# Optimization experiments

Hardware: AMD Instinct MI355X
Metric: run time of the kernel (lower is better)

Reference implementation:

```python
import jax, jax.numpy as jnp
import numpy as np

B, T, S, D, H, DK = 2, 2048, 2048, 1024, 16, 64


def setup_inputs() -> dict:
    key = jax.random.key(0)
    ks = jax.random.split(key, 11)
    s = 1.0 / np.sqrt(D)
    return {
        "query": jax.random.normal(ks[0], (B, T, D), jnp.float32),
        "value": jax.random.normal(ks[1], (B, S, D), jnp.float32),
        "key": jax.random.normal(ks[2], (B, S, D), jnp.float32),
        "Wq": jax.random.normal(ks[3], (D, H, DK), jnp.float32) * s,
        "bq": jnp.zeros((H, DK), jnp.float32),
        "Wk": jax.random.normal(ks[4], (D, H, DK), jnp.float32) * s,
        "bk": jnp.zeros((H, DK), jnp.float32),
        "Wv": jax.random.normal(ks[5], (D, H, DK), jnp.float32) * s,
        "bv": jnp.zeros((H, DK), jnp.float32),
        "Wo": jax.random.normal(ks[6], (H, DK, D), jnp.float32) * (1.0 / np.sqrt(H * DK)),
        "bo": jnp.zeros((D,), jnp.float32),
    }


def reference(query, value, key, Wq, bq, Wk, bk, Wv, bv, Wo, bo):
    # Projections: (B, seq, D) x (D, H, DK) -> (B, seq, H, DK)
    q = jnp.einsum("btd,dhk->bthk", query, Wq) + bq
    k = jnp.einsum("bsd,dhk->bshk", key, Wk) + bk
    v = jnp.einsum("bsd,dhk->bshk", value, Wv) + bv
    # Scaled dot-product attention (keras scales query by 1/sqrt(key_dim))
    q = q * (1.0 / np.sqrt(DK)).astype(np.float32)
    scores = jnp.einsum("bshk,bthk->bhts", k, q)  # (B, H, T, S)
    probs = jax.nn.softmax(scores, axis=-1)
    attn = jnp.einsum("bhts,bshk->bthk", probs, v)  # (B, T, H, DK)
    # Output projection back to model dim
    out = jnp.einsum("bthk,hkd->btd", attn, Wo) + bo
    return out
```

## Files before the change

kernel.cpp:

```cpp
#include <hip/hip_runtime.h>
#include <math.h>

#define BB  2
#define TT  2048
#define SSQ 2048
#define DD  1024
#define HH  16
#define DKK 64
#define MM  (BB*TT)
#define NN  (HH*DKK)

typedef __attribute__((ext_vector_type(8))) short short8;
typedef __attribute__((ext_vector_type(4))) float f32x4;

__device__ __forceinline__ short f2bf(float x) {
    unsigned u = __builtin_bit_cast(unsigned, x);
    unsigned r = (u + 0x7FFFu + ((u >> 16) & 1u)) >> 16;
    return (short)r;
}

__device__ __forceinline__ void glds16(const void* g, void* l) {
    __builtin_amdgcn_global_load_lds(
        (const __attribute__((address_space(1))) void*)g,
        (__attribute__((address_space(3))) void*)l, 16, 0, 0);
}

__global__ __launch_bounds__(256)
void to_bf16_acts(const float* __restrict__ a0, const float* __restrict__ a1,
                  const float* __restrict__ a2,
                  short* __restrict__ o0, short* __restrict__ o1,
                  short* __restrict__ o2)
{
    int z = blockIdx.y;
    const float* in = (z == 0) ? a0 : (z == 1) ? a1 : a2;
    short* out = (z == 0) ? o0 : (z == 1) ? o1 : o2;
    size_t i0 = ((size_t)blockIdx.x * 256 + threadIdx.x) * 8;
    f32x4 f0 = *(const f32x4*)(in + i0);
    f32x4 f1 = *(const f32x4*)(in + i0 + 4);
    short8 v;
#pragma unroll
    for (int j = 0; j < 4; j++) v[j] = f2bf(f0[j]);
#pragma unroll
    for (int j = 0; j < 4; j++) v[4 + j] = f2bf(f1[j]);
    *(short8*)(out + i0) = v;
}

__global__ __launch_bounds__(256)
void wtrans(const float* __restrict__ w0, const float* __restrict__ w1,
            const float* __restrict__ w2, const float* __restrict__ w3,
            short* __restrict__ t0, short* __restrict__ t1,
            short* __restrict__ t2, short* __restrict__ t3)
{
    __shared__ float Ls[64][65];
    int z = blockIdx.z;
    const float* in = (z == 0) ? w0 : (z == 1) ? w1 : (z == 2) ? w2 : w3;
    short* out = (z == 0) ? t0 : (z == 1) ? t1 : (z == 2) ? t2 : t3;
    const int r0 = blockIdx.y * 64, c0 = blockIdx.x * 64;
    const int t = threadIdx.x;
    const int r = t >> 2, c4 = t & 3;

    const float* src = in + (size_t)(r0 + r) * DD + c0 + c4 * 16;
#pragma unroll
    for (int i = 0; i < 4; i++) {
        f32x4 f = *(const f32x4*)(src + i * 4);
#pragma unroll
        for (int j = 0; j < 4; j++) Ls[r][c4 * 16 + i * 4 + j] = f[j];
    }
    __syncthreads();

    short8 va, vb;
#pragma unroll
    for (int j = 0; j < 8; j++) va[j] = f2bf(Ls[c4 * 16 + j][r]);
#pragma unroll
    for (int j = 0; j < 8; j++) vb[j] = f2bf(Ls[c4 * 16 + 8 + j][r]);
    short* dst = out + (size_t)(c0 + r) * DD + r0 + c4 * 16;
    *(short8*)dst = va;
    *(short8*)(dst + 8) = vb;
}

__global__ __launch_bounds__(256)
void vtrans(const short* __restrict__ in, short* __restrict__ out)
{
    __shared__ short Ls[64][72];
    const int bh = blockIdx.y;
    const int t0 = blockIdx.x * 64;
    const int tid = threadIdx.x;
    const int r = tid >> 2, c4 = tid & 3;

    const short* src = in + ((size_t)bh * TT + t0 + r) * DKK + c4 * 16;
    *(short8*)&Ls[r][c4 * 16]     = *(const short8*)(src);
    *(short8*)&Ls[r][c4 * 16 + 8] = *(const short8*)(src + 8);
    __syncthreads();

    short8 a, b;
#pragma unroll
    for (int j = 0; j < 8; j++) a[j] = Ls[c4 * 16 + j][r];
#pragma unroll
    for (int j = 0; j < 8; j++) b[j] = Ls[c4 * 16 + 8 + j][r];
    short* dst = out + ((size_t)bh * DKK + r) * SSQ + t0 + c4 * 16;
    *(short8*)dst = a;
    *(short8*)(dst + 8) = b;
}

__device__ __forceinline__ void gemm_core(const short* __restrict__ A,
                                          const short* __restrict__ Bt,
                                          int m0, int n0,
                                          short* As, short* Bs,
                                          f32x4 (&acc)[4][4])
{
    const int tid = threadIdx.x;
    const int w = tid >> 6, l = tid & 63;
    const int l15 = l & 15, quad = l >> 4;
    const int wm = w >> 1, wn = w & 1;

#pragma unroll
    for (int i = 0; i < 4; i++)
#pragma unroll
        for (int j = 0; j < 4; j++) acc[i][j] = (f32x4){0.f, 0.f, 0.f, 0.f};

    const int r = tid >> 2, cseg = tid & 3;
    const short* gA = A + (size_t)(m0 + r) * DD + cseg * 8;
    const short* gB = Bt + (size_t)(n0 + r) * DD + cseg * 8;
    short* ldsA = As + w * 512;
    short* ldsB = Bs + w * 512;

    for (int k0 = 0; k0 < DD; k0 += 32) {
        glds16(gA + k0,                 ldsA);
        glds16(gA + (size_t)64 * DD + k0, ldsA + 2048);
        glds16(gB + k0,                 ldsB);
        glds16(gB + (size_t)64 * DD + k0, ldsB + 2048);
        __syncthreads();

        short8 bF[4];
#pragma unroll
        for (int ni = 0; ni < 4; ni++)
            bF[ni] = *(const short8*)&Bs[(wn * 64 + ni * 16 + l15) * 32 + quad * 8];
#pragma unroll
        for (int mi = 0; mi < 4; mi++) {
            short8 aF = *(const short8*)&As[(wm * 64 + mi * 16 + l15) * 32 + quad * 8];
#pragma unroll
            for (int ni = 0; ni < 4; ni++)
                acc[mi][ni] = __builtin_amdgcn_mfma_f32_16x16x32_bf16(aF, bF[ni], acc[mi][ni], 0, 0, 0);
        }
        __syncthreads();
    }
}

__global__ __launch_bounds__(256, 3)
void gemm_qkv(const short* __restrict__ Aq, const short* __restrict__ Ak,
              const short* __restrict__ Av,
              const short* __restrict__ Wqt, const short* __restrict__ Wkt,
              const short* __restrict__ Wvt,
              const float* __restrict__ bq, const float* __restrict__ bk,
              const float* __restrict__ bv,
              short* __restrict__ Qb, short* __restrict__ Kb,
              short* __restrict__ Vtmp)
{
    __shared__ short As[128 * 32];
    __shared__ short Bs[128 * 32];
    const int z = blockIdx.z;
    const short* A  = (z == 0) ? Aq : (z == 1) ? Ak : Av;
    const short* Bt = (z == 0) ? Wqt : (z == 1) ? Wkt : Wvt;
    const float* bias = (z == 0) ? bq : (z == 1) ? bk : bv;
    short* dst = (z == 0) ? Qb : (z == 1) ? Kb : Vtmp;
    const int m0 = blockIdx.y * 128, n0 = blockIdx.x * 128;

    f32x4 acc[4][4];
    gemm_core(A, Bt, m0, n0, As, Bs, acc);

    const int tid = threadIdx.x;
    const int w = tid >> 6, l = tid & 63;
    const int l15 = l & 15, quad = l >> 4;
    const int wm = w >> 1, wn = w & 1;
    const float scale = (z == 0) ? 0.1803368801f : 1.0f;

#pragma unroll
    for (int mi = 0; mi < 4; mi++) {
#pragma unroll
        for (int reg = 0; reg < 4; reg++) {
            int m = m0 + wm * 64 + mi * 16 + quad * 4 + reg;
            int b = m >> 11, t = m & 2047;
#pragma unroll
            for (int ni = 0; ni < 4; ni++) {
                int n = n0 + wn * 64 + ni * 16 + l15;
                float vv = (acc[mi][ni][reg] + bias[n]) * scale;
                int h = n >> 6, dk = n & 63;
                dst[((size_t)(b * HH + h) * TT + t) * DKK + dk] = f2bf(vv);
            }
        }
    }
}

__global__ __launch_bounds__(256, 3)
void gemm_out(const short* __restrict__ Ab, const short* __restrict__ Wot,
              const float* __restrict__ bo, float* __restrict__ out)
{
    __shared__ short As[128 * 32];
    __shared__ short Bs[128 * 32];
    const int m0 = blockIdx.y * 128, n0 = blockIdx.x * 128;

    f32x4 acc[4][4];
    gemm_core(Ab, Wot, m0, n0, As, Bs, acc);

    const int tid = threadIdx.x;
    const int w = tid >> 6, l = tid & 63;
    const int l15 = l & 15, quad = l >> 4;
    const int wm = w >> 1, wn = w & 1;

#pragma unroll
    for (int mi = 0; mi < 4; mi++) {
#pragma unroll
        for (int reg = 0; reg < 4; reg++) {
            int m = m0 + wm * 64 + mi * 16 + quad * 4 + reg;
#pragma unroll
            for (int ni = 0; ni < 4; ni++) {
                int n = n0 + wn * 64 + ni * 16 + l15;
                out[(size_t)m * DD + n] = acc[mi][ni][reg] + bo[n];
            }
        }
    }
}

__global__ __launch_bounds__(256, 2)
void attn_mfma(const short* __restrict__ Qb, const short* __restrict__ Kb,
               const short* __restrict__ Vbt, short* __restrict__ Ab)
{
    __shared__ short QPs[128 * 72];
    __shared__ short Ks[64 * 72];
    __shared__ short Vs[64 * 72];

    const int tid = threadIdx.x;
    const int w = tid >> 6, l = tid & 63;
    const int l15 = l & 15, quad = l >> 4;
    const int bh = blockIdx.y;
    const int t0 = blockIdx.x * 128;
    const size_t hb = (size_t)bh * SSQ * DKK;
    const int r = tid >> 2, c4 = tid & 3;

    {
        int r2 = tid >> 1, half = tid & 1;
        const short* g = Qb + hb + (size_t)(t0 + r2) * 64 + half * 32;
        short* s = QPs + r2 * 72 + half * 32;
        *(short8*)(s + 0)  = *(const short8*)(g + 0);
        *(short8*)(s + 8)  = *(const short8*)(g + 8);
        *(short8*)(s + 16) = *(const short8*)(g + 16);
        *(short8*)(s + 24) = *(const short8*)(g + 24);
    }
    __threadfence_block();
    short8 qf[2][2];
#pragma unroll
    for (int mf = 0; mf < 2; mf++)
#pragma unroll
        for (int kk = 0; kk < 2; kk++)
            qf[mf][kk] = *(const short8*)&QPs[(32 * w + 16 * mf + l15) * 72 + kk * 32 + quad * 8];

    const short* gkb = Kb + hb + (size_t)r * 64 + c4 * 16;
    const short* gvb = Vbt + hb + (size_t)r * SSQ + c4 * 16;
    short8 kr0 = *(const short8*)(gkb + 0);
    short8 kr1 = *(const short8*)(gkb + 8);
    short8 vr0 = *(const short8*)(gvb + 0);
    short8 vr1 = *(const short8*)(gvb + 8);

    f32x4 o[2][4];
#pragma unroll
    for (int mf = 0; mf < 2; mf++)
#pragma unroll
        for (int j = 0; j < 4; j++) o[mf][j] = (f32x4){0.f, 0.f, 0.f, 0.f};
    float lsum[2][4];
#pragma unroll
    for (int mf = 0; mf < 2; mf++)
#pragma unroll
        for (int j = 0; j < 4; j++) lsum[mf][j] = 0.f;

    short* sk = Ks + r * 72 + c4 * 16;
    short* sv = Vs + r * 72 + c4 * 16;

    for (int s0 = 0; s0 < SSQ; s0 += 64) {
        __syncthreads();
        *(short8*)(sk + 0) = kr0;
        *(short8*)(sk + 8) = kr1;
        *(short8*)(sv + 0) = vr0;
        *(short8*)(sv + 8) = vr1;
        if (s0 + 64 < SSQ) {
            const short* gk = gkb + (size_t)(s0 + 64) * 64;
            const short* gv = gvb + (s0 + 64);
            kr0 = *(const short8*)(gk + 0);
            kr1 = *(const short8*)(gk + 8);
            vr0 = *(const short8*)(gv + 0);
            vr1 = *(const short8*)(gv + 8);
        }
        __syncthreads();

        f32x4 sc[2][4];
#pragma unroll
        for (int mf = 0; mf < 2; mf++)
#pragma unroll
            for (int j = 0; j < 4; j++) sc[mf][j] = (f32x4){0.f, 0.f, 0.f, 0.f};
#pragma unroll
        for (int kk = 0; kk < 2; kk++) {
#pragma unroll
            for (int np = 0; np < 4; np++) {
                short8 bK = *(const short8*)&Ks[(16 * np + l15) * 72 + kk * 32 + quad * 8];
                sc[0][np] = __builtin_amdgcn_mfma_f32_16x16x32_bf16(qf[0][kk], bK, sc[0][np], 0, 0, 0);
                sc[1][np] = __builtin_amdgcn_mfma_f32_16x16x32_bf16(qf[1][kk], bK, sc[1][np], 0, 0, 0);
            }
        }

#pragma unroll
        for (int mf = 0; mf < 2; mf++) {
            int prow = (32 * w + 16 * mf + quad * 4) * 72 + l15;
#pragma unroll
            for (int reg = 0; reg < 4; reg++) {
                int pr = prow + reg * 72;
#pragma unroll
                for (int np = 0; np < 4; np++) {
                    float p = __builtin_amdgcn_exp2f(sc[mf][np][reg]);
                    QPs[pr + 16 * np] = (short)(__builtin_bit_cast(unsigned, p) >> 16);
                    lsum[mf][reg] += p;
                }
            }
        }
        __threadfence_block();

#pragma unroll
        for (int kk = 0; kk < 2; kk++) {
            short8 aP0 = *(const short8*)&QPs[(32 * w + l15) * 72 + kk * 32 + quad * 8];
            short8 aP1 = *(const short8*)&QPs[(32 * w + 16 + l15) * 72 + kk * 32 + quad * 8];
#pragma unroll
            for (int np = 0; np < 4; np++) {
                short8 bV = *(const short8*)&Vs[(16 * np + l15) * 72 + kk * 32 + quad * 8];
                o[0][np] = __builtin_amdgcn_mfma_f32_16x16x32_bf16(aP0, bV, o[0][np], 0, 0, 0);
                o[1][np] = __builtin_amdgcn_mfma_f32_16x16x32_bf16(aP1, bV, o[1][np], 0, 0, 0);
            }
        }
    }

    const int b = bh >> 4, h = bh & 15;
#pragma unroll
    for (int mf = 0; mf < 2; mf++) {
#pragma unroll
        for (int reg = 0; reg < 4; reg++) {
            float ls = lsum[mf][reg];
            ls += __shfl_xor(ls, 1);
            ls += __shfl_xor(ls, 2);
            ls += __shfl_xor(ls, 4);
            ls += __shfl_xor(ls, 8);
            float inv = 1.f / ls;
            int t = t0 + 32 * w + 16 * mf + quad * 4 + reg;
#pragma unroll
            for (int np = 0; np < 4; np++) {
                Ab[((size_t)(b * TT + t) * HH + h) * DKK + 16 * np + l15] =
                    f2bf(o[mf][np][reg] * inv);
            }
        }
    }
}

extern "C" void kernel_launch(void* const* d_in, const int* in_sizes, int n_in,
                              void* d_out, int out_size, void* d_ws, size_t ws_size,
                              hipStream_t stream)
{
    const float* query = (const float*)d_in[0];
    const float* value = (const float*)d_in[1];
    const float* key   = (const float*)d_in[2];
    const float* Wq    = (const float*)d_in[3];
    const float* bq    = (const float*)d_in[4];
    const float* Wk    = (const float*)d_in[5];
    const float* bk    = (const float*)d_in[6];
    const float* Wv    = (const float*)d_in[7];
    const float* bv    = (const float*)d_in[8];
    const float* Wo    = (const float*)d_in[9];
    const float* bo    = (const float*)d_in[10];
    float* out = (float*)d_out;

    const size_t actE = (size_t)MM * DD;
    const size_t wE   = (size_t)DD * NN;
    short* p = (short*)d_ws;
    short* Aq   = p; p += actE;
    short* Ak   = p; p += actE;
    short* Av   = p; p += actE;
    short* Wqt  = p; p += wE;
    short* Wkt  = p; p += wE;
    short* Wvt  = p; p += wE;
    short* Wot  = p; p += wE;
    short* Qb   = p; p += actE;
    short* Kb   = p; p += actE;
    short* Vtmp = p; p += actE;
    short* Vbt  = p; p += actE;
    short* Ab   = p; p += actE;

    dim3 blk(256);

    to_bf16_acts<<<dim3((unsigned)(actE / 2048), 3), blk, 0, stream>>>(
        query, key, value, Aq, Ak, Av);

    wtrans<<<dim3(16, 16, 4), blk, 0, stream>>>(Wq, Wk, Wv, Wo, Wqt, Wkt, Wvt, Wot);

    gemm_qkv<<<dim3(NN / 128, MM / 128, 3), blk, 0, stream>>>(
        Aq, Ak, Av, Wqt, Wkt, Wvt, bq, bk, bv, Qb, Kb, Vtmp);

    vtrans<<<dim3(TT / 64, BB * HH), blk, 0, stream>>>(Vtmp, Vbt);

    attn_mfma<<<dim3(TT / 128, BB * HH), blk, 0, stream>>>(Qb, Kb, Vbt, Ab);

    gemm_out<<<dim3(DD / 128, MM / 128), blk, 0, stream>>>(Ab, Wot, bo, out);
}
```

Measured before the change: 240.9 us.

## Widen attention KV tile to 128 and use 128x64 tiles for output GEMM

The attention kernel now stages 128 keys and values per iteration instead of 64. This halves the number of barrier-separated loop trips and doubles the K dimension of the P·V MFMA chain, at the cost of more LDS and register pressure. The output projection GEMM switches from 128x128 tiles to 128x64 tiles with its own inlined direct-to-LDS load loop, launching twice as many blocks to fill more CUs. The new layout keeps global loads staged through registers without multi-buffering, so load latency is still only partly hidden.

```diff
diff --git a/kernel.cpp b/kernel.cpp
--- a/kernel.cpp
+++ b/kernel.cpp
@@ -191,30 +191,57 @@
     }
 }
 
-__global__ __launch_bounds__(256, 3)
+__global__ __launch_bounds__(256, 2)
 void gemm_out(const short* __restrict__ Ab, const short* __restrict__ Wot,
               const float* __restrict__ bo, float* __restrict__ out)
 {
     __shared__ short As[128 * 32];
-    __shared__ short Bs[128 * 32];
-    const int m0 = blockIdx.y * 128, n0 = blockIdx.x * 128;
-
-    f32x4 acc[4][4];
-    gemm_core(Ab, Wot, m0, n0, As, Bs, acc);
-
+    __shared__ short Bs[64 * 32];
+    const int m0 = blockIdx.y * 128, n0 = blockIdx.x * 64;
     const int tid = threadIdx.x;
     const int w = tid >> 6, l = tid & 63;
     const int l15 = l & 15, quad = l >> 4;
-    const int wm = w >> 1, wn = w & 1;
-
-#pragma unroll
-    for (int mi = 0; mi < 4; mi++) {
+
+    f32x4 acc[2][4];
+#pragma unroll
+    for (int i = 0; i < 2; i++)
+#pragma unroll
+        for (int j = 0; j < 4; j++) acc[i][j] = (f32x4){0.f, 0.f, 0.f, 0.f};
+
+    const int r = tid >> 2, cseg = tid & 3;
+    const short* gA = Ab + (size_t)(m0 + r) * DD + cseg * 8;
+    const short* gB = Wot + (size_t)(n0 + r) * DD + cseg * 8;
+    short* ldsA = As + w * 512;
+    short* ldsB = Bs + w * 512;
+
+    for (int k0 = 0; k0 < DD; k0 += 32) {
+        glds16(gA + k0,                   ldsA);
+        glds16(gA + (size_t)64 * DD + k0, ldsA + 2048);
+        glds16(gB + k0,                   ldsB);
+        __syncthreads();
+
+        short8 bF[4];
+#pragma unroll
+        for (int ni = 0; ni < 4; ni++)
+            bF[ni] = *(const short8*)&Bs[(ni * 16 + l15) * 32 + quad * 8];
+#pragma unroll
+        for (int mi = 0; mi < 2; mi++) {
+            short8 aF = *(const short8*)&As[(w * 32 + mi * 16 + l15) * 32 + quad * 8];
+#pragma unroll
+            for (int ni = 0; ni < 4; ni++)
+                acc[mi][ni] = __builtin_amdgcn_mfma_f32_16x16x32_bf16(aF, bF[ni], acc[mi][ni], 0, 0, 0);
+        }
+        __syncthreads();
+    }
+
+#pragma unroll
+    for (int mi = 0; mi < 2; mi++) {
 #pragma unroll
         for (int reg = 0; reg < 4; reg++) {
-            int m = m0 + wm * 64 + mi * 16 + quad * 4 + reg;
+            int m = m0 + w * 32 + mi * 16 + quad * 4 + reg;
 #pragma unroll
             for (int ni = 0; ni < 4; ni++) {
-                int n = n0 + wn * 64 + ni * 16 + l15;
+                int n = n0 + ni * 16 + l15;
                 out[(size_t)m * DD + n] = acc[mi][ni][reg] + bo[n];
             }
         }
@@ -225,9 +252,9 @@
 void attn_mfma(const short* __restrict__ Qb, const short* __restrict__ Kb,
                const short* __restrict__ Vbt, short* __restrict__ Ab)
 {
-    __shared__ short QPs[128 * 72];
-    __shared__ short Ks[64 * 72];
-    __shared__ short Vs[64 * 72];
+    __shared__ short QPs[128 * 132];
+    __shared__ short Ks[128 * 68];
+    __shared__ short Vs[64 * 132];
 
     const int tid = threadIdx.x;
     const int w = tid >> 6, l = tid & 63;
@@ -235,12 +262,11 @@
     const int bh = blockIdx.y;
     const int t0 = blockIdx.x * 128;
     const size_t hb = (size_t)bh * SSQ * DKK;
-    const int r = tid >> 2, c4 = tid & 3;
 
     {
         int r2 = tid >> 1, half = tid & 1;
         const short* g = Qb + hb + (size_t)(t0 + r2) * 64 + half * 32;
-        short* s = QPs + r2 * 72 + half * 32;
+        short* s = QPs + r2 * 132 + half * 32;
         *(short8*)(s + 0)  = *(const short8*)(g + 0);
         *(short8*)(s + 8)  = *(const short8*)(g + 8);
         *(short8*)(s + 16) = *(const short8*)(g + 16);
@@ -252,14 +278,21 @@
     for (int mf = 0; mf < 2; mf++)
 #pragma unroll
         for (int kk = 0; kk < 2; kk++)
-            qf[mf][kk] = *(const short8*)&QPs[(32 * w + 16 * mf + l15) * 72 + kk * 32 + quad * 8];
-
-    const short* gkb = Kb + hb + (size_t)r * 64 + c4 * 16;
-    const short* gvb = Vbt + hb + (size_t)r * SSQ + c4 * 16;
-    short8 kr0 = *(const short8*)(gkb + 0);
-    short8 kr1 = *(const short8*)(gkb + 8);
-    short8 vr0 = *(const short8*)(gvb + 0);
-    short8 vr1 = *(const short8*)(gvb + 8);
+            qf[mf][kk] = *(const short8*)&QPs[(32 * w + 16 * mf + l15) * 132 + kk * 32 + quad * 8];
+
+    const int rk = tid >> 1, kseg = (tid & 1) * 32;
+    const int rv = tid >> 2, vseg = (tid & 3) * 32;
+    const short* gkb = Kb + hb + (size_t)rk * 64 + kseg;
+    const short* gvb = Vbt + hb + (size_t)rv * SSQ + vseg;
+    short* sk = Ks + rk * 68 + kseg;
+    short* sv = Vs + rv * 132 + vseg;
+
+    short8 kr[4], vr[4];
+#pragma unroll
+    for (int i = 0; i < 4; i++) {
+        kr[i] = *(const short8*)(gkb + i * 8);
+        vr[i] = *(const short8*)(gvb + i * 8);
+    }
 
     f32x4 o[2][4];
 #pragma unroll
@@ -272,65 +305,66 @@
 #pragma unroll
         for (int j = 0; j < 4; j++) lsum[mf][j] = 0.f;
 
-    short* sk = Ks + r * 72 + c4 * 16;
-    short* sv = Vs + r * 72 + c4 * 16;
-
-    for (int s0 = 0; s0 < SSQ; s0 += 64) {
-        __syncthreads();
-        *(short8*)(sk + 0) = kr0;
-        *(short8*)(sk + 8) = kr1;
-        *(short8*)(sv + 0) = vr0;
-        *(short8*)(sv + 8) = vr1;
-        if (s0 + 64 < SSQ) {
-            const short* gk = gkb + (size_t)(s0 + 64) * 64;
-            const short* gv = gvb + (s0 + 64);
-            kr0 = *(const short8*)(gk + 0);
-            kr1 = *(const short8*)(gk + 8);
-            vr0 = *(const short8*)(gv + 0);
-            vr1 = *(const short8*)(gv + 8);
-        }
-        __syncthreads();
-
-        f32x4 sc[2][4];
-#pragma unroll
-        for (int mf = 0; mf < 2; mf++)
-#pragma unroll
-            for (int j = 0; j < 4; j++) sc[mf][j] = (f32x4){0.f, 0.f, 0.f, 0.f};
-#pragma unroll
-        for (int kk = 0; kk < 2; kk++) {
-#pragma unroll
-            for (int np = 0; np < 4; np++) {
-                short8 bK = *(const short8*)&Ks[(16 * np + l15) * 72 + kk * 32 + quad * 8];
-                sc[0][np] = __builtin_amdgcn_mfma_f32_16x16x32_bf16(qf[0][kk], bK, sc[0][np], 0, 0, 0);
-                sc[1][np] = __builtin_amdgcn_mfma_f32_16x16x32_bf16(qf[1][kk], bK, sc[1][np], 0, 0, 0);
-            }
-        }
-
-#pragma unroll
-        for (int mf = 0; mf < 2; mf++) {
-            int prow = (32 * w + 16 * mf + quad * 4) * 72 + l15;
-#pragma unroll
-            for (int reg = 0; reg < 4; reg++) {
-                int pr = prow + reg * 72;
+    for (int s0 = 0; s0 < SSQ; s0 += 128) {
+        __syncthreads();
+#pragma unroll
+        for (int i = 0; i < 4; i++) {
+            *(short8*)(sk + i * 8) = kr[i];
+            *(short8*)(sv + i * 8) = vr[i];
+        }
+        if (s0 + 128 < SSQ) {
+            const short* gk = gkb + (size_t)(s0 + 128) * 64;
+            const short* gv = gvb + (s0 + 128);
+#pragma unroll
+            for (int i = 0; i < 4; i++) {
+                kr[i] = *(const short8*)(gk + i * 8);
+                vr[i] = *(const short8*)(gv + i * 8);
+            }
+        }
+        __syncthreads();
+
+#pragma unroll
+        for (int sh = 0; sh < 2; sh++) {
+            f32x4 sc[2][4];
+#pragma unroll
+            for (int mf = 0; mf < 2; mf++)
+#pragma unroll
+                for (int j = 0; j < 4; j++) sc[mf][j] = (f32x4){0.f, 0.f, 0.f, 0.f};
+#pragma unroll
+            for (int kk = 0; kk < 2; kk++) {
 #pragma unroll
                 for (int np = 0; np < 4; np++) {
-                    float p = __builtin_amdgcn_exp2f(sc[mf][np][reg]);
-                    QPs[pr + 16 * np] = (short)(__builtin_bit_cast(unsigned, p) >> 16);
-                    lsum[mf][reg] += p;
+                    short8 bK = *(const short8*)&Ks[(sh * 64 + 16 * np + l15) * 68 + kk * 32 + quad * 8];
+                    sc[0][np] = __builtin_amdgcn_mfma_f32_16x16x32_bf16(qf[0][kk], bK, sc[0][np], 0, 0, 0);
+                    sc[1][np] = __builtin_amdgcn_mfma_f32_16x16x32_bf16(qf[1][kk], bK, sc[1][np], 0, 0, 0);
                 }
             }
+#pragma unroll
+            for (int mf = 0; mf < 2; mf++) {
+                int prow = (32 * w + 16 * mf + quad * 4) * 132 + sh * 64 + l15;
+#pragma unroll
+                for (int reg = 0; reg < 4; reg++) {
+                    int pr = prow + reg * 132;
+#pragma unroll
+                    for (int np = 0; np < 4; np++) {
+                        float p = __builtin_amdgcn_exp2f(sc[mf][np][reg]);
+                        QPs[pr + 16 * np] = (short)(__builtin_bit_cast(unsigned, p) >> 16);
+                        lsum[mf][reg] += p;
+                    }
+                }
+            }
         }
         __threadfence_block();
 
 #pragma unroll
-        for (int kk = 0; kk < 2; kk++) {
-            short8 aP0 = *(const short8*)&QPs[(32 * w + l15) * 72 + kk * 32 + quad * 8];
-            short8 aP1 = *(const short8*)&QPs[(32 * w + 16 + l15) * 72 + kk * 32 + quad * 8];
-#pragma unroll
-            for (int np = 0; np < 4; np++) {
-                short8 bV = *(const short8*)&Vs[(16 * np + l15) * 72 + kk * 32 + quad * 8];
-                o[0][np] = __builtin_amdgcn_mfma_f32_16x16x32_bf16(aP0, bV, o[0][np], 0, 0, 0);
-                o[1][np] = __builtin_amdgcn_mfma_f32_16x16x32_bf16(aP1, bV, o[1][np], 0, 0, 0);
+        for (int kk = 0; kk < 4; kk++) {
+            short8 aP0 = *(const short8*)&QPs[(32 * w + l15) * 132 + kk * 32 + quad * 8];
+            short8 aP1 = *(const short8*)&QPs[(32 * w + 16 + l15) * 132 + kk * 32 + quad * 8];
+#pragma unroll
+            for (int nf = 0; nf < 4; nf++) {
+                short8 bV = *(const short8*)&Vs[(16 * nf + l15) * 132 + kk * 32 + quad * 8];
+                o[0][nf] = __builtin_amdgcn_mfma_f32_16x16x32_bf16(aP0, bV, o[0][nf], 0, 0, 0);
+                o[1][nf] = __builtin_amdgcn_mfma_f32_16x16x32_bf16(aP1, bV, o[1][nf], 0, 0, 0);
             }
         }
     }
@@ -348,9 +382,9 @@
             float inv = 1.f / ls;
             int t = t0 + 32 * w + 16 * mf + quad * 4 + reg;
 #pragma unroll
-            for (int np = 0; np < 4; np++) {
-                Ab[((size_t)(b * TT + t) * HH + h) * DKK + 16 * np + l15] =
-                    f2bf(o[mf][np][reg] * inv);
+            for (int nf = 0; nf < 4; nf++) {
+                Ab[((size_t)(b * TT + t) * HH + h) * DKK + 16 * nf + l15] =
+                    f2bf(o[mf][nf][reg] * inv);
             }
         }
     }
@@ -403,5 +437,5 @@
 
     attn_mfma<<<dim3(TT / 128, BB * HH), blk, 0, stream>>>(Qb, Kb, Vbt, Ab);
 
-    gemm_out<<<dim3(DD / 128, MM / 128), blk, 0, stream>>>(Ab, Wot, bo, out);
-}
+    gemm_out<<<dim3(DD / 64, MM / 128), blk, 0, stream>>>(Ab, Wot, bo, out);
+}
```

Measured after the change: 254.0 us. 5.5% more time.
